# Optimization experiments

Measured on AMD Instinct MI355X. Metric: run time of the kernel, lower is better.

Reference implementation:

```python
import jax, jax.numpy as jnp
import numpy as np

B, S, D, H = 2, 2048, 2048, 16
HD = D // H  # head_dim = 128


def setup_inputs() -> dict:
    key = jax.random.key(0)
    ks = jax.random.split(key, 5)
    scale = 1.0 / np.sqrt(D)
    return {
        "x": jax.random.normal(ks[0], (B, S, D), dtype=jnp.float32),
        "Wq": jax.random.normal(ks[1], (D, D), dtype=jnp.float32) * scale,
        "Wk": jax.random.normal(ks[2], (D, D), dtype=jnp.float32) * scale,
        "Wv": jax.random.normal(ks[3], (D, D), dtype=jnp.float32) * scale,
        "Wo": jax.random.normal(ks[4], (D, D), dtype=jnp.float32) * scale,
    }


def reference(x, Wq, Wk, Wv, Wo):
    # torch Linear: y = x @ W.T (weight is [out, in], no bias)
    b, s, d = x.shape
    def split_heads(t):
        return t.reshape(b, s, H, HD).transpose(0, 2, 1, 3)  # [B,H,S,HD]
    q = split_heads(x @ Wq.T)
    k = split_heads(x @ Wk.T)
    v = split_heads(x @ Wv.T)
    scores = jnp.einsum("bhqd,bhkd->bhqk", q, k) / jnp.sqrt(jnp.float32(HD))
    attn = jax.nn.softmax(scores, axis=-1)
    out = jnp.einsum("bhqk,bhkd->bhqd", attn, v)  # [B,H,S,HD]
    out = out.transpose(0, 2, 1, 3).reshape(b, s, d)
    return out @ Wo.T
```

## Files before the change

### kernel.cpp

```cpp
#include <hip/hip_runtime.h>
#include <stdint.h>

typedef unsigned short u16t;
typedef short bf16x8 __attribute__((ext_vector_type(8)));
typedef float f32x4 __attribute__((ext_vector_type(4)));

#define B_ 2
#define S_ 2048
#define D_ 2048
#define H_ 16
#define HD_ 128

#define MFMA16(a,b,c) __builtin_amdgcn_mfma_f32_16x16x32_bf16((a),(b),(c),0,0,0)

typedef const __attribute__((address_space(1))) void* gptr_t;
typedef __attribute__((address_space(3))) void* lptr_t;
#define GLL16(src, dst) __builtin_amdgcn_global_load_lds((gptr_t)(src), (lptr_t)(dst), 16, 0, 0)

__device__ __forceinline__ u16t f2bf(float f) {
  uint32_t u = __builtin_bit_cast(uint32_t, f);
  u = (u + 0x7fffu + ((u >> 16) & 1u)) >> 16;
  return (u16t)u;
}

__global__ void cvt5_kernel(const float* __restrict__ x,
                            const float* __restrict__ w0, const float* __restrict__ w1,
                            const float* __restrict__ w2, const float* __restrict__ w3,
                            u16t* xo, u16t* o0, u16t* o1, u16t* o2, u16t* o3) {
  int blk = blockIdx.x;
  const float* in; u16t* out; int i;
  if (blk < 4096) { in = x; out = xo; i = blk * 256 + threadIdx.x; }
  else {
    int b2 = blk - 4096;
    int wsel = b2 >> 11;
    in  = (wsel == 0) ? w0 : (wsel == 1) ? w1 : (wsel == 2) ? w2 : w3;
    out = (wsel == 0) ? o0 : (wsel == 1) ? o1 : (wsel == 2) ? o2 : o3;
    i = (b2 & 2047) * 256 + threadIdx.x;
  }
  const float4* p = (const float4*)in + (size_t)i * 2;
  float4 a = p[0], b = p[1];
  union { u16t u[8]; uint4 v; } pk;
  pk.u[0]=f2bf(a.x); pk.u[1]=f2bf(a.y); pk.u[2]=f2bf(a.z); pk.u[3]=f2bf(a.w);
  pk.u[4]=f2bf(b.x); pk.u[5]=f2bf(b.y); pk.u[6]=f2bf(b.z); pk.u[7]=f2bf(b.w);
  *(uint4*)(out + (size_t)i * 8) = pk.v;
}

template<int MODE>
__global__ __launch_bounds__(512, 2) void gemm256(const u16t* __restrict__ A,
                                                  const u16t* __restrict__ Bw0,
                                                  const u16t* __restrict__ Bw1,
                                                  const u16t* __restrict__ Bw2,
                                                  void* __restrict__ C0,
                                                  void* __restrict__ C1,
                                                  void* __restrict__ C2,
                                                  int Mtiles, int Ntiles, int tpw,
                                                  int K, float a0, float a1, float a2) {
  __shared__ __attribute__((aligned(16))) u16t Al[2][2][128*64];
  __shared__ __attribute__((aligned(16))) u16t Bl[2][2][128*64];
  int nwg = Mtiles * Ntiles;
  int bid = blockIdx.x;
  int wg  = ((bid & 7) * (nwg >> 3)) + (bid >> 3);
  int mt = wg / Ntiles, nt = wg % Ntiles;
  int wsel = nt / tpw;
  const u16t* Bw = (wsel == 0) ? Bw0 : (wsel == 1) ? Bw1 : Bw2;
  const u16t* Ag = A  + (size_t)mt * 256 * K;
  const u16t* Bg = Bw + (size_t)(nt - wsel*tpw) * 256 * K;

  int t = threadIdx.x, lane = t & 63, w = t >> 6;
  int wm = w >> 2, wn = w & 3;
  int c = lane & 15, g = lane >> 4;

  auto stageA = [&](int buf, int hf, int kt) {
    #pragma unroll
    for (int j = 0; j < 2; j++) {
      int s = j*512 + t;
      int row = s >> 3;
      int ks = (s & 7) ^ (row & 7);
      GLL16(Ag + (size_t)(hf*128 + row) * K + kt*64 + ks*8,
            &Al[buf][hf][(j*512 + (t & ~63)) * 8]);
    }
  };
  auto stageB = [&](int buf, int hf, int kt) {
    #pragma unroll
    for (int j = 0; j < 2; j++) {
      int s = j*512 + t;
      int row = s >> 3;
      int ks = (s & 7) ^ (row & 7);
      GLL16(Bg + (size_t)(hf*128 + row) * K + kt*64 + ks*8,
            &Bl[buf][hf][(j*512 + (t & ~63)) * 8]);
    }
  };

  f32x4 acc[8][4];
  #pragma unroll
  for (int mf = 0; mf < 8; mf++)
    #pragma unroll
    for (int nf = 0; nf < 4; nf++) acc[mf][nf] = (f32x4){0.f,0.f,0.f,0.f};

  int sOf[2];
  #pragma unroll
  for (int ks = 0; ks < 2; ks++) sOf[ks] = (((ks*4 + g) ^ (c & 7)) << 3);
  int arow = c * 64;
  int brow = (wn & 1) * 4096 + c * 64;

  bf16x8 Af[8][2], Bf[4][2];
  auto RD_A = [&](int p, int mf0) {
    #pragma unroll
    for (int mq = 0; mq < 4; mq++)
      #pragma unroll
      for (int ks = 0; ks < 2; ks++)
        Af[mf0+mq][ks] = *(const bf16x8*)&Al[p][wm][(mf0+mq)*1024 + arow + sOf[ks]];
  };
  auto RD_B = [&](int p, int nf0) {
    #pragma unroll
    for (int nq = 0; nq < 2; nq++)
      #pragma unroll
      for (int ks = 0; ks < 2; ks++)
        Bf[nf0+nq][ks] = *(const bf16x8*)&Bl[p][wn >> 1][(nf0+nq)*1024 + brow + sOf[ks]];
  };
  auto quad = [&](int MF0, int NF0) {
    __builtin_amdgcn_s_setprio(1);
    #pragma unroll
    for (int mq = 0; mq < 4; mq++)
      #pragma unroll
      for (int nq = 0; nq < 2; nq++)
        #pragma unroll
        for (int ks = 0; ks < 2; ks++)
          acc[MF0+mq][NF0+nq] = MFMA16(Af[MF0+mq][ks], Bf[NF0+nq][ks], acc[MF0+mq][NF0+nq]);
    __builtin_amdgcn_s_setprio(0);
  };
  #define BAR() __builtin_amdgcn_s_barrier()
  #define LGKM0() asm volatile("s_waitcnt lgkmcnt(0)" ::: "memory")

  int nk = K >> 6;
  stageA(0,0,0); stageA(0,1,0); stageB(0,0,0); stageB(0,1,0);
  stageA(1,0,1);
  asm volatile("s_waitcnt vmcnt(2)" ::: "memory");
  BAR();

  for (int it = 0; it < nk/2; ++it) {
    int t1 = 2*it + 1, tn0 = 2*it + 2, tn1 = 2*it + 3;
    bool st = tn0 < nk;
    RD_A(0,0); RD_B(0,0);
    stageA(1,1,t1);
    BAR(); LGKM0(); quad(0,0); BAR();
    RD_B(0,2);
    stageB(1,0,t1);
    BAR(); LGKM0(); quad(0,2); BAR();
    RD_A(0,4);
    stageB(1,1,t1);
    BAR(); LGKM0(); quad(4,0); BAR();
    if (st) { stageA(0,0,tn0); asm volatile("s_waitcnt vmcnt(2)" ::: "memory"); }
    else    {                  asm volatile("s_waitcnt vmcnt(0)" ::: "memory"); }
    BAR(); quad(4,2); BAR();
    RD_A(1,0); RD_B(1,0);
    if (st) stageA(0,1,tn0);
    BAR(); LGKM0(); quad(0,0); BAR();
    RD_B(1,2);
    if (st) stageB(0,0,tn0);
    BAR(); LGKM0(); quad(0,2); BAR();
    RD_A(1,4);
    if (st) stageB(0,1,tn0);
    BAR(); LGKM0(); quad(4,0); BAR();
    if (st) { stageA(1,0,tn1); asm volatile("s_waitcnt vmcnt(2)" ::: "memory"); }
    BAR(); quad(4,2); BAR();
  }
  #undef BAR
  #undef LGKM0

  float alpha = (wsel == 0) ? a0 : (wsel == 1) ? a1 : a2;
  int m0 = mt*256 + wm*128 + 4*g;
  int n0 = (nt - wsel*tpw)*256 + wn*64 + c;
  if (MODE == 0) {
    float* C = (float*)C0;
    #pragma unroll
    for (int mf = 0; mf < 8; mf++)
      #pragma unroll
      for (int nf = 0; nf < 4; nf++)
        #pragma unroll
        for (int r = 0; r < 4; r++)
          C[(size_t)(m0 + 16*mf + r) * D_ + n0 + 16*nf] = acc[mf][nf][r] * alpha;
  } else if (wsel != 2) {
    u16t* C = (u16t*)((wsel == 0) ? C0 : C1);
    #pragma unroll
    for (int mf = 0; mf < 8; mf++)
      #pragma unroll
      for (int nf = 0; nf < 4; nf++)
        #pragma unroll
        for (int r = 0; r < 4; r++)
          C[(size_t)(m0 + 16*mf + r) * D_ + n0 + 16*nf] = f2bf(acc[mf][nf][r] * alpha);
  } else {
    u16t* Vt = (u16t*)C2;
    #pragma unroll
    for (int mf = 0; mf < 8; mf++) {
      int m = m0 + 16*mf;
      int rowb = (m >> 11) << 11;
      int colb = m & 2047;
      #pragma unroll
      for (int nf = 0; nf < 4; nf++) {
        union { u16t u[4]; uint2 v; } pk;
        #pragma unroll
        for (int r = 0; r < 4; r++) pk.u[r] = f2bf(acc[mf][nf][r] * alpha);
        *(uint2*)&Vt[(size_t)(rowb + n0 + 16*nf) * 2048 + colb] = pk.v;
      }
    }
  }
}

__global__ __launch_bounds__(256, 2) void attn_kernel(const u16t* __restrict__ Q,
                                                      const u16t* __restrict__ Kg,
                                                      const u16t* __restrict__ Vt,
                                                      u16t* __restrict__ O) {
  __shared__ __attribute__((aligned(16))) u16t Kl[2][64*128];
  __shared__ __attribute__((aligned(16))) u16t Vl[2][128*64];
  __shared__ __attribute__((aligned(16))) u16t Pl[4][32*64];
  int bid = blockIdx.x;
  int qt = bid & 15, head = bid >> 4;
  int b = head >> 4, h = head & 15;
  int t = threadIdx.x, lane = t & 63, w = t >> 6;
  int c = lane & 15, g = lane >> 4;
  int q0 = qt*128 + w*32;

  bf16x8 qf[2][4];
  #pragma unroll
  for (int mi = 0; mi < 2; mi++)
    #pragma unroll
    for (int ks = 0; ks < 4; ks++)
      qf[mi][ks] = *(const bf16x8*)&Q[(size_t)(b*S_ + q0 + c + 16*mi)*D_ + h*HD_ + 8*g + 32*ks];

  f32x4 oacc[8][2];
  #pragma unroll
  for (int mf = 0; mf < 8; mf++) { oacc[mf][0] = (f32x4){0,0,0,0}; oacc[mf][1] = (f32x4){0,0,0,0}; }
  f32x4 lacc[2];
  lacc[0] = (f32x4){0,0,0,0}; lacc[1] = (f32x4){0,0,0,0};
  bf16x8 ones;
  #pragma unroll
  for (int j = 0; j < 8; j++) ones[j] = (short)0x3F80;

  auto stageK = [&](int buf, int kt) {
    int s0 = kt*64;
    #pragma unroll
    for (int i = 0; i < 4; i++) {
      int row = (i*256 + t) >> 4;
      int xs = (t & 15) ^ (row & 15);
      GLL16(&Kg[(size_t)(b*S_ + s0 + row)*D_ + h*HD_ + xs*8], &Kl[buf][(i*256 + (t & ~63))*8]);
    }
  };
  auto stageV = [&](int buf, int kt) {
    int s0 = kt*64;
    #pragma unroll
    for (int i = 0; i < 4; i++) {
      int d = (i*256 + t) >> 3;
      int xs = (t & 7) ^ (d & 7);
      GLL16(&Vt[(size_t)(head*HD_ + d)*S_ + s0 + xs*8], &Vl[buf][(i*256 + (t & ~63))*8]);
    }
  };

  stageK(0, 0); stageV(0, 0);
  int cur = 0;
  for (int kt = 0; kt < 32; ++kt) {
    __syncthreads();
    if (kt + 1 < 32) { stageK(cur ^ 1, kt + 1); stageV(cur ^ 1, kt + 1); }

    f32x4 sacc[2][4];
    #pragma unroll
    for (int mi = 0; mi < 2; mi++)
      #pragma unroll
      for (int nf = 0; nf < 4; nf++) sacc[mi][nf] = (f32x4){0,0,0,0};
    #pragma unroll
    for (int ks = 0; ks < 4; ks++) {
      #pragma unroll
      for (int nf = 0; nf < 4; nf++) {
        bf16x8 kf = *(const bf16x8*)&Kl[cur][(c + 16*nf)*128 + (((g + 4*ks) ^ c) & 15)*8];
        sacc[0][nf] = MFMA16(qf[0][ks], kf, sacc[0][nf]);
        sacc[1][nf] = MFMA16(qf[1][ks], kf, sacc[1][nf]);
      }
    }

    #pragma unroll
    for (int mi = 0; mi < 2; mi++)
      #pragma unroll
      for (int nf = 0; nf < 4; nf++)
        #pragma unroll
        for (int reg = 0; reg < 4; reg++) {
          float p = __expf(sacc[mi][nf][reg]);
          int r = 16*mi + 4*g + reg;
          int col = c + 16*nf;
          Pl[w][r*64 + ((((col >> 3) ^ (r & 7)) & 7) << 3) + (col & 7)] = f2bf(p);
        }

    #pragma unroll
    for (int ks = 0; ks < 2; ks++) {
      int ps = ((g + 4*ks) ^ (c & 7)) & 7;
      bf16x8 pf0 = *(const bf16x8*)&Pl[w][(c      )*64 + ps*8];
      bf16x8 pf1 = *(const bf16x8*)&Pl[w][(c + 16 )*64 + ps*8];
      lacc[0] = MFMA16(ones, pf0, lacc[0]);
      lacc[1] = MFMA16(ones, pf1, lacc[1]);
      #pragma unroll
      for (int mf = 0; mf < 8; mf++) {
        bf16x8 vf = *(const bf16x8*)&Vl[cur][(c + 16*mf)*64 + ps*8];
        oacc[mf][0] = MFMA16(vf, pf0, oacc[mf][0]);
        oacc[mf][1] = MFMA16(vf, pf1, oacc[mf][1]);
      }
    }
    cur ^= 1;
  }

  float li0 = 1.f / lacc[0][0];
  float li1 = 1.f / lacc[1][0];
  #pragma unroll
  for (int mf = 0; mf < 8; mf++) {
    #pragma unroll
    for (int nf = 0; nf < 2; nf++) {
      float liv = nf ? li1 : li0;
      union { u16t u[4]; uint2 v; } pk;
      #pragma unroll
      for (int r = 0; r < 4; r++) pk.u[r] = f2bf(oacc[mf][nf][r] * liv);
      int qrow = q0 + c + 16*nf;
      int d0 = 16*mf + 4*g;
      *(uint2*)&O[(size_t)(b*S_ + qrow)*D_ + h*HD_ + d0] = pk.v;
    }
  }
}

extern "C" void kernel_launch(void* const* d_in, const int* in_sizes, int n_in,
                              void* d_out, int out_size, void* d_ws, size_t ws_size,
                              hipStream_t stream) {
  const float* x  = (const float*)d_in[0];
  const float* Wq = (const float*)d_in[1];
  const float* Wk = (const float*)d_in[2];
  const float* Wv = (const float*)d_in[3];
  const float* Wo = (const float*)d_in[4];

  const size_t M1 = 1024*1024;
  u16t* ws  = (u16t*)d_ws;
  u16t* xb  = ws;
  u16t* Wqb = xb  + 8*M1;
  u16t* Wkb = Wqb + 4*M1;
  u16t* Wvb = Wkb + 4*M1;
  u16t* Wob = Wvb + 4*M1;
  u16t* Qb  = Wob + 4*M1;
  u16t* Vtb = (u16t*)d_out;
  u16t* Kb  = (u16t*)d_out + 8*M1;
  u16t* AOb = Wqb;

  const float scl = 0.08838834764831845f;

  cvt5_kernel<<<12288, 256, 0, stream>>>(x, Wq, Wk, Wv, Wo, xb, Wqb, Wkb, Wvb, Wob);

  gemm256<1><<<384, 512, 0, stream>>>(xb, Wqb, Wkb, Wvb, Qb, Kb, Vtb,
                                      16, 24, 8, 2048, scl, 1.0f, 1.0f);

  attn_kernel<<<512, 256, 0, stream>>>(Qb, Kb, Vtb, AOb);

  gemm256<0><<<128, 512, 0, stream>>>(AOb, Wob, Wob, Wob, d_out, d_out, d_out,
                                      16, 8, 8, 2048, 1.0f, 1.0f, 1.0f);
}
```

Measured before the change: 407.5 us.

## Switch GEMM to 256x128 tiles with simple double-buffered K loop

Shrinks each GEMM workgroup's N tile from 256 to 128, so the QKV projection launches 768 blocks and the output projection 256. The 8 waves are rearranged into a 4x2 grid with 64x64 per-wave tiles. The hand-interleaved half-tile staging schedule is replaced by a plain two-stage double buffer: each iteration waits on vmcnt, does one barrier, reads all fragments, and issues the next prefetch between two MFMA halves. More blocks should fill more CUs and the simpler loop needs fewer barriers, at the cost of less operand reuse per block and a lower occupancy hint in launch_bounds.

```diff
diff --git a/kernel.cpp b/kernel.cpp
--- a/kernel.cpp
+++ b/kernel.cpp
@@ -46,7 +46,7 @@
 }
 
 template<int MODE>
-__global__ __launch_bounds__(512, 2) void gemm256(const u16t* __restrict__ A,
+__global__ __launch_bounds__(512, 1) void gemm256(const u16t* __restrict__ A,
                                                   const u16t* __restrict__ Bw0,
                                                   const u16t* __restrict__ Bw1,
                                                   const u16t* __restrict__ Bw2,
@@ -55,8 +55,8 @@
                                                   void* __restrict__ C2,
                                                   int Mtiles, int Ntiles, int tpw,
                                                   int K, float a0, float a1, float a2) {
-  __shared__ __attribute__((aligned(16))) u16t Al[2][2][128*64];
-  __shared__ __attribute__((aligned(16))) u16t Bl[2][2][128*64];
+  __shared__ __attribute__((aligned(16))) u16t Al[2][256*64];
+  __shared__ __attribute__((aligned(16))) u16t Bl[2][128*64];
   int nwg = Mtiles * Ntiles;
   int bid = blockIdx.x;
   int wg  = ((bid & 7) * (nwg >> 3)) + (bid >> 3);
@@ -64,117 +64,95 @@
   int wsel = nt / tpw;
   const u16t* Bw = (wsel == 0) ? Bw0 : (wsel == 1) ? Bw1 : Bw2;
   const u16t* Ag = A  + (size_t)mt * 256 * K;
-  const u16t* Bg = Bw + (size_t)(nt - wsel*tpw) * 256 * K;
+  const u16t* Bg = Bw + (size_t)(nt - wsel*tpw) * 128 * K;
 
   int t = threadIdx.x, lane = t & 63, w = t >> 6;
-  int wm = w >> 2, wn = w & 3;
+  int wm = w >> 1, wn = w & 1;
   int c = lane & 15, g = lane >> 4;
 
-  auto stageA = [&](int buf, int hf, int kt) {
+  auto stageA = [&](int buf, int kt) {
+    #pragma unroll
+    for (int j = 0; j < 4; j++) {
+      int s = j*512 + t;
+      int row = s >> 3;
+      int ks = (s & 7) ^ (row & 7);
+      GLL16(Ag + (size_t)row * K + kt*64 + ks*8, &Al[buf][(j*512 + (t & ~63)) * 8]);
+    }
+  };
+  auto stageB = [&](int buf, int kt) {
     #pragma unroll
     for (int j = 0; j < 2; j++) {
       int s = j*512 + t;
       int row = s >> 3;
       int ks = (s & 7) ^ (row & 7);
-      GLL16(Ag + (size_t)(hf*128 + row) * K + kt*64 + ks*8,
-            &Al[buf][hf][(j*512 + (t & ~63)) * 8]);
-    }
-  };
-  auto stageB = [&](int buf, int hf, int kt) {
-    #pragma unroll
-    for (int j = 0; j < 2; j++) {
-      int s = j*512 + t;
-      int row = s >> 3;
-      int ks = (s & 7) ^ (row & 7);
-      GLL16(Bg + (size_t)(hf*128 + row) * K + kt*64 + ks*8,
-            &Bl[buf][hf][(j*512 + (t & ~63)) * 8]);
-    }
-  };
-
-  f32x4 acc[8][4];
-  #pragma unroll
-  for (int mf = 0; mf < 8; mf++)
+      GLL16(Bg + (size_t)row * K + kt*64 + ks*8, &Bl[buf][(j*512 + (t & ~63)) * 8]);
+    }
+  };
+
+  f32x4 acc[4][4];
+  #pragma unroll
+  for (int mf = 0; mf < 4; mf++)
     #pragma unroll
     for (int nf = 0; nf < 4; nf++) acc[mf][nf] = (f32x4){0.f,0.f,0.f,0.f};
 
   int sOf[2];
   #pragma unroll
   for (int ks = 0; ks < 2; ks++) sOf[ks] = (((ks*4 + g) ^ (c & 7)) << 3);
-  int arow = c * 64;
-  int brow = (wn & 1) * 4096 + c * 64;
-
-  bf16x8 Af[8][2], Bf[4][2];
-  auto RD_A = [&](int p, int mf0) {
-    #pragma unroll
-    for (int mq = 0; mq < 4; mq++)
+  int arow = (wm*64 + c) * 64;
+  int brow = (wn*64 + c) * 64;
+
+  bf16x8 Af[4][2], Bf[4][2];
+  auto RD_ALL = [&](int p) {
+    #pragma unroll
+    for (int mf = 0; mf < 4; mf++)
       #pragma unroll
       for (int ks = 0; ks < 2; ks++)
-        Af[mf0+mq][ks] = *(const bf16x8*)&Al[p][wm][(mf0+mq)*1024 + arow + sOf[ks]];
-  };
-  auto RD_B = [&](int p, int nf0) {
-    #pragma unroll
-    for (int nq = 0; nq < 2; nq++)
+        Af[mf][ks] = *(const bf16x8*)&Al[p][arow + mf*1024 + sOf[ks]];
+    #pragma unroll
+    for (int nf = 0; nf < 4; nf++)
       #pragma unroll
       for (int ks = 0; ks < 2; ks++)
-        Bf[nf0+nq][ks] = *(const bf16x8*)&Bl[p][wn >> 1][(nf0+nq)*1024 + brow + sOf[ks]];
-  };
-  auto quad = [&](int MF0, int NF0) {
+        Bf[nf][ks] = *(const bf16x8*)&Bl[p][brow + nf*1024 + sOf[ks]];
+  };
+  auto quad = [&](int MF0) {
     __builtin_amdgcn_s_setprio(1);
     #pragma unroll
-    for (int mq = 0; mq < 4; mq++)
-      #pragma unroll
-      for (int nq = 0; nq < 2; nq++)
+    for (int mq = 0; mq < 2; mq++)
+      #pragma unroll
+      for (int nf = 0; nf < 4; nf++)
         #pragma unroll
         for (int ks = 0; ks < 2; ks++)
-          acc[MF0+mq][NF0+nq] = MFMA16(Af[MF0+mq][ks], Bf[NF0+nq][ks], acc[MF0+mq][NF0+nq]);
+          acc[MF0+mq][nf] = MFMA16(Af[MF0+mq][ks], Bf[nf][ks], acc[MF0+mq][nf]);
     __builtin_amdgcn_s_setprio(0);
   };
-  #define BAR() __builtin_amdgcn_s_barrier()
+  #define BARM()  asm volatile("s_barrier" ::: "memory")
   #define LGKM0() asm volatile("s_waitcnt lgkmcnt(0)" ::: "memory")
 
   int nk = K >> 6;
-  stageA(0,0,0); stageA(0,1,0); stageB(0,0,0); stageB(0,1,0);
-  stageA(1,0,1);
-  asm volatile("s_waitcnt vmcnt(2)" ::: "memory");
-  BAR();
-
-  for (int it = 0; it < nk/2; ++it) {
-    int t1 = 2*it + 1, tn0 = 2*it + 2, tn1 = 2*it + 3;
-    bool st = tn0 < nk;
-    RD_A(0,0); RD_B(0,0);
-    stageA(1,1,t1);
-    BAR(); LGKM0(); quad(0,0); BAR();
-    RD_B(0,2);
-    stageB(1,0,t1);
-    BAR(); LGKM0(); quad(0,2); BAR();
-    RD_A(0,4);
-    stageB(1,1,t1);
-    BAR(); LGKM0(); quad(4,0); BAR();
-    if (st) { stageA(0,0,tn0); asm volatile("s_waitcnt vmcnt(2)" ::: "memory"); }
-    else    {                  asm volatile("s_waitcnt vmcnt(0)" ::: "memory"); }
-    BAR(); quad(4,2); BAR();
-    RD_A(1,0); RD_B(1,0);
-    if (st) stageA(0,1,tn0);
-    BAR(); LGKM0(); quad(0,0); BAR();
-    RD_B(1,2);
-    if (st) stageB(0,0,tn0);
-    BAR(); LGKM0(); quad(0,2); BAR();
-    RD_A(1,4);
-    if (st) stageB(0,1,tn0);
-    BAR(); LGKM0(); quad(4,0); BAR();
-    if (st) { stageA(1,0,tn1); asm volatile("s_waitcnt vmcnt(2)" ::: "memory"); }
-    BAR(); quad(4,2); BAR();
-  }
-  #undef BAR
+  stageA(0,0); stageB(0,0); stageA(1,1); stageB(1,1);
+
+  for (int kt = 0; kt < nk; ++kt) {
+    int p = kt & 1;
+    if (kt < nk - 1) asm volatile("s_waitcnt vmcnt(6)" ::: "memory");
+    else             asm volatile("s_waitcnt vmcnt(0)" ::: "memory");
+    BARM();
+    RD_ALL(p);
+    quad(0);
+    LGKM0();
+    BARM();
+    if (kt + 2 < nk) { stageA(p, kt + 2); stageB(p, kt + 2); }
+    quad(2);
+  }
+  #undef BARM
   #undef LGKM0
 
   float alpha = (wsel == 0) ? a0 : (wsel == 1) ? a1 : a2;
-  int m0 = mt*256 + wm*128 + 4*g;
-  int n0 = (nt - wsel*tpw)*256 + wn*64 + c;
+  int m0 = mt*256 + wm*64 + 4*g;
+  int n0 = (nt - wsel*tpw)*128 + wn*64 + c;
   if (MODE == 0) {
     float* C = (float*)C0;
     #pragma unroll
-    for (int mf = 0; mf < 8; mf++)
+    for (int mf = 0; mf < 4; mf++)
       #pragma unroll
       for (int nf = 0; nf < 4; nf++)
         #pragma unroll
@@ -183,7 +161,7 @@
   } else if (wsel != 2) {
     u16t* C = (u16t*)((wsel == 0) ? C0 : C1);
     #pragma unroll
-    for (int mf = 0; mf < 8; mf++)
+    for (int mf = 0; mf < 4; mf++)
       #pragma unroll
       for (int nf = 0; nf < 4; nf++)
         #pragma unroll
@@ -192,7 +170,7 @@
   } else {
     u16t* Vt = (u16t*)C2;
     #pragma unroll
-    for (int mf = 0; mf < 8; mf++) {
+    for (int mf = 0; mf < 4; mf++) {
       int m = m0 + 16*mf;
       int rowb = (m >> 11) << 11;
       int colb = m & 2047;
@@ -348,11 +326,11 @@
 
   cvt5_kernel<<<12288, 256, 0, stream>>>(x, Wq, Wk, Wv, Wo, xb, Wqb, Wkb, Wvb, Wob);
 
-  gemm256<1><<<384, 512, 0, stream>>>(xb, Wqb, Wkb, Wvb, Qb, Kb, Vtb,
-                                      16, 24, 8, 2048, scl, 1.0f, 1.0f);
+  gemm256<1><<<768, 512, 0, stream>>>(xb, Wqb, Wkb, Wvb, Qb, Kb, Vtb,
+                                      16, 48, 16, 2048, scl, 1.0f, 1.0f);
 
   attn_kernel<<<512, 256, 0, stream>>>(Qb, Kb, Vtb, AOb);
 
-  gemm256<0><<<128, 512, 0, stream>>>(AOb, Wob, Wob, Wob, d_out, d_out, d_out,
-                                      16, 8, 8, 2048, 1.0f, 1.0f, 1.0f);
-}
+  gemm256<0><<<256, 512, 0, stream>>>(AOb, Wob, Wob, Wob, d_out, d_out, d_out,
+                                      16, 16, 16, 2048, 1.0f, 1.0f, 1.0f);
+}
```

Result: faster. 375.3 us (-7.9%).
